# Performance work log

Hardware: AMD Instinct MI355X
Metric: run time of the kernel (lower is better)

## Reference

```python
import jax, jax.numpy as jnp
import numpy as np

D_MODEL = 1024
N_HEADS = 16
HEAD_DIM = D_MODEL // N_HEADS  # 64; used only as softmax scale in windowed path
WINDOW = 128


def _window_starts(seq_len, window):
    # Faithful to the torch loop: stride = window//2, last window right-aligned.
    starts = []
    for i in range(0, seq_len, window // 2):
        end = min(i + window, seq_len)
        starts.append(max(0, end - window))
        if end == seq_len:
            break
    return np.asarray(starts, dtype=np.int32)


def setup_inputs() -> dict:
    key = jax.random.key(0)
    ks = jax.random.split(key, 9)
    B, S = 4, 4096
    sc = 1.0 / np.sqrt(D_MODEL)
    return {
        "x": jax.random.normal(ks[0], (B, S, D_MODEL), jnp.float32),
        "Wq": jax.random.normal(ks[1], (D_MODEL, D_MODEL), jnp.float32) * sc,
        "bq": jax.random.normal(ks[2], (D_MODEL,), jnp.float32) * 0.02,
        "Wk": jax.random.normal(ks[3], (D_MODEL, D_MODEL), jnp.float32) * sc,
        "bk": jax.random.normal(ks[4], (D_MODEL,), jnp.float32) * 0.02,
        "Wv": jax.random.normal(ks[5], (D_MODEL, D_MODEL), jnp.float32) * sc,
        "bv": jax.random.normal(ks[6], (D_MODEL,), jnp.float32) * 0.02,
        "Wo": jax.random.normal(ks[7], (D_MODEL, D_MODEL), jnp.float32) * sc,
        "bo": jax.random.normal(ks[8], (D_MODEL,), jnp.float32) * 0.02,
    }


def reference(x, Wq, bq, Wk, bk, Wv, bv, Wo, bo):
    B, S, D = x.shape
    q = x @ Wq + bq  # [B,S,D]
    k = x @ Wk + bk
    v = x @ Wv + bv

    # Overlapping sliding windows (heads merged, as in the original windowed path).
    starts = _window_starts(S, WINDOW)                      # [W]
    idx = starts[:, None] + np.arange(WINDOW)[None, :]      # [W, w] static
    idx_j = jnp.asarray(idx)
    qw = q[:, idx_j]  # [B, W, w, D]
    kw = k[:, idx_j]
    vw = v[:, idx_j]
    scores = jnp.einsum('bwqd,bwkd->bwqk', qw, kw) / np.sqrt(HEAD_DIM)
    attn = jax.nn.softmax(scores, axis=-1)
    out_w = jnp.einsum('bwqk,bwkd->bwqd', attn, vw)         # [B, W, w, D]

    # Overlap-add then average by coverage counts.
    flat_idx = idx.reshape(-1)
    out = jnp.zeros((B, S, D), x.dtype).at[:, flat_idx].add(
        out_w.reshape(B, -1, D))
    counts = jnp.zeros((S,), x.dtype).at[flat_idx].add(1.0)
    out = out / counts[None, :, None]

    return out @ Wo + bo
```

## Files before the change

### kernel.cpp

```cpp
#include <hip/hip_runtime.h>
#include <stdint.h>
#include <stddef.h>

#define D_MODEL 1024
#define SEQ     4096
#define BATCH   4
#define MTOT    (BATCH*SEQ)
#define NWIN    63

typedef __bf16 bf16;
typedef __bf16 bf16x8 __attribute__((ext_vector_type(8)));
typedef __bf16 bf16x4 __attribute__((ext_vector_type(4)));
typedef float  floatx4 __attribute__((ext_vector_type(4)));

__device__ __forceinline__ void async_ld16(const void* g, void* l) {
  __builtin_amdgcn_global_load_lds(
      (const __attribute__((address_space(1))) unsigned int*)g,
      (__attribute__((address_space(3))) unsigned int*)l,
      16, 0, 0);
}


__global__ __launch_bounds__(256)
void cvt_x_kernel(const float* __restrict__ x, bf16* __restrict__ xb)
{
  const int i = blockIdx.x * 256 + threadIdx.x;
  const float4 v = ((const float4*)x)[i];
  bf16x4 o = { (bf16)v.x, (bf16)v.y, (bf16)v.z, (bf16)v.w };
  ((bf16x4*)xb)[i] = o;
}

__global__ __launch_bounds__(256)
void cvt_wt_kernel(const float* __restrict__ W0, const float* __restrict__ W1,
                   const float* __restrict__ W2, const float* __restrict__ W3,
                   bf16* __restrict__ wt)
{
  __shared__ float tile[32][33];
  const float* Wsel = (blockIdx.z == 0) ? W0 : (blockIdx.z == 1) ? W1
                    : (blockIdx.z == 2) ? W2 : W3;
  bf16* Wt = wt + (size_t)blockIdx.z * D_MODEL * D_MODEL;
  const int tx = threadIdx.x & 31, ty = threadIdx.x >> 5;
  const int tn = blockIdx.x * 32, tk = blockIdx.y * 32;
#pragma unroll
  for (int j = 0; j < 32; j += 8)
    tile[ty + j][tx] = Wsel[(size_t)(tk + ty + j) * D_MODEL + (tn + tx)];
  __syncthreads();
#pragma unroll
  for (int j = 0; j < 32; j += 8)
    Wt[(size_t)(tn + ty + j) * D_MODEL + (tk + tx)] = (bf16)tile[tx][ty + j];
}

__device__ __forceinline__ void stage_tile(const bf16* __restrict__ Ab,
                                           const bf16* __restrict__ Bb,
                                           bf16* As, bf16* Bs, int t, int buf,
                                           int w, int l)
{
  const int k0 = t << 5;
  bf16* Ad = As + buf * 8192;
  bf16* Bd = Bs + buf * 8192;
#pragma unroll
  for (int i = 0; i < 2; ++i) {
    const int f = w * 2 + i;
    async_ld16(Ab + (size_t)(f * 16) * D_MODEL + k0, Ad + f * 512 + l * 8);
    async_ld16(Bb + (size_t)(f * 16) * D_MODEL + k0, Bd + f * 512 + l * 8);
  }
}

__device__ __forceinline__ void gemm_core_256(const bf16* __restrict__ A,
                                              const bf16* __restrict__ Bt,
                                              int m0, int n0,
                                              bf16* As, bf16* Bs,
                                              floatx4 (&acc)[8][4],
                                              int w, int l)
{
  const int ll = l & 15, lh = l >> 4;
  const int wm = w >> 2, wn = w & 3;
  const bf16* Ab = A  + (size_t)(m0 + ll) * D_MODEL + lh * 8;
  const bf16* Bb = Bt + (size_t)(n0 + ll) * D_MODEL + lh * 8;

  stage_tile(Ab, Bb, As, Bs, 0, 0, w, l);
  stage_tile(Ab, Bb, As, Bs, 1, 1, w, l);

  for (int t = 0; t < 32; ++t) {
    if (t < 31) asm volatile("s_waitcnt vmcnt(4)" ::: "memory");
    else        asm volatile("s_waitcnt vmcnt(0)" ::: "memory");
    __builtin_amdgcn_s_barrier();
    __builtin_amdgcn_sched_barrier(0);
    const bf16* Ac = As + (t & 1) * 8192;
    const bf16* Bc = Bs + (t & 1) * 8192;
    bf16x8 af[8], bfr[4];
#pragma unroll
    for (int mt = 0; mt < 8; ++mt)
      af[mt]  = *(const bf16x8*)&Ac[(wm * 8 + mt) * 512 + l * 8];
#pragma unroll
    for (int nt = 0; nt < 4; ++nt)
      bfr[nt] = *(const bf16x8*)&Bc[(wn * 4 + nt) * 512 + l * 8];
    __builtin_amdgcn_s_setprio(1);
#pragma unroll
    for (int mt = 0; mt < 8; ++mt)
#pragma unroll
      for (int nt = 0; nt < 4; ++nt)
        acc[mt][nt] = __builtin_amdgcn_mfma_f32_16x16x32_bf16(af[mt], bfr[nt], acc[mt][nt], 0, 0, 0);
    __builtin_amdgcn_s_setprio(0);
    __builtin_amdgcn_sched_barrier(0);
    __builtin_amdgcn_s_barrier();
    __builtin_amdgcn_sched_barrier(0);
    if (t + 2 < 32) stage_tile(Ab, Bb, As, Bs, t + 2, t & 1, w, l);
  }
}

__global__ __launch_bounds__(512, 2)
void gemm_qkv(const bf16* __restrict__ A, const bf16* __restrict__ Bt,
              const float* __restrict__ bq, const float* __restrict__ bk,
              const float* __restrict__ bv,
              bf16* __restrict__ qo, bf16* __restrict__ ko, bf16* __restrict__ vto)
{
  __shared__ __attribute__((aligned(16))) bf16 As[16384];
  __shared__ __attribute__((aligned(16))) bf16 Bs[16384];
  const int tid = threadIdx.x;
  const int w = tid >> 6, l = tid & 63;
  const int ll = l & 15, lh = l >> 4;
  const int wm = w >> 2, wn = w & 3;

  const int idx = blockIdx.x;
  const int xcd = idx & 7;
  const int local = idx >> 3;
  const int msub = local & 7;
  const int nblk = local >> 3;
  const int mblk = xcd * 8 + msub;
  const int m0 = mblk * 256, n0 = nblk * 256;

  floatx4 acc[8][4];
#pragma unroll
  for (int i = 0; i < 8; ++i)
#pragma unroll
    for (int j = 0; j < 4; ++j) acc[i][j] = (floatx4)0.f;

  gemm_core_256(A, Bt, m0, n0, As, Bs, acc, w, l);

  const int sel = n0 >> 10;
  const int ncl = n0 & 1023;
  const float* bias = (sel == 0) ? bq : (sel == 1) ? bk : bv;

#pragma unroll
  for (int mt = 0; mt < 8; ++mt) {
#pragma unroll
    for (int nt = 0; nt < 4; ++nt) {
      const int colL = ncl + wn * 64 + nt * 16 + ll;
      const float bvv = bias[colL];
#pragma unroll
      for (int r = 0; r < 4; ++r) {
        const int row = m0 + wm * 128 + mt * 16 + lh * 4 + r;
        const float v = acc[mt][nt][r] + bvv;
        if (sel == 0) {
          qo[(size_t)row * D_MODEL + colL] = (bf16)v;
        } else if (sel == 1) {
          ko[(size_t)row * D_MODEL + colL] = (bf16)v;
        } else {
          const int bb = row >> 12, s = row & 4095;
          vto[((size_t)bb * D_MODEL + colL) * SEQ + s] = (bf16)v;
        }
      }
    }
  }
}

__global__ __launch_bounds__(512, 2)
void gemm_out(const bf16* __restrict__ A, const bf16* __restrict__ Bt,
              const float* __restrict__ bias, float* __restrict__ C)
{
  __shared__ __attribute__((aligned(16))) bf16 As[16384];
  __shared__ __attribute__((aligned(16))) bf16 Bs[16384];
  const int tid = threadIdx.x;
  const int w = tid >> 6, l = tid & 63;
  const int ll = l & 15, lh = l >> 4;
  const int wm = w >> 2, wn = w & 3;

  const int idx = blockIdx.x;
  const int xcd = idx & 7;
  const int local = idx >> 3;
  const int msub = local & 7;
  const int nblk = local >> 3;
  const int mblk = xcd * 8 + msub;
  const int m0 = mblk * 256, n0 = nblk * 256;

  floatx4 acc[8][4];
#pragma unroll
  for (int i = 0; i < 8; ++i)
#pragma unroll
    for (int j = 0; j < 4; ++j) acc[i][j] = (floatx4)0.f;

  gemm_core_256(A, Bt, m0, n0, As, Bs, acc, w, l);

#pragma unroll
  for (int mt = 0; mt < 8; ++mt) {
#pragma unroll
    for (int nt = 0; nt < 4; ++nt) {
      const int col = n0 + wn * 64 + nt * 16 + ll;
      const float bvv = bias[col];
#pragma unroll
      for (int r = 0; r < 4; ++r) {
        const int row = m0 + wm * 128 + mt * 16 + lh * 4 + r;
        C[(size_t)row * D_MODEL + col] = acc[mt][nt][r] + bvv;
      }
    }
  }
}

__global__ __launch_bounds__(256)
void qk_softmax(const bf16* __restrict__ qb, const bf16* __restrict__ kb,
                bf16* __restrict__ Pg)
{
  __shared__ __attribute__((aligned(16))) bf16 As[8192];
  __shared__ __attribute__((aligned(16))) bf16 Bs[16384];
  __shared__ float redM[4][64];
  __shared__ float redS[4][64];

  const int tid = threadIdx.x;
  const int w = tid >> 6, l = tid & 63, ll = l & 15, lh = l >> 4;
  const int wh = blockIdx.x;
  const int win = wh >> 1, half = wh & 1;
  const int b = blockIdx.y;

  const bf16* Aq = qb + ((size_t)b * SEQ + win * 64 + half * 64) * D_MODEL
                 + (size_t)ll * D_MODEL + lh * 8;
  const bf16* Ak = kb + ((size_t)b * SEQ + win * 64) * D_MODEL
                 + (size_t)ll * D_MODEL + lh * 8;

  floatx4 acc[4][2];
#pragma unroll
  for (int i = 0; i < 4; ++i)
#pragma unroll
    for (int j = 0; j < 2; ++j) acc[i][j] = (floatx4)0.f;

  auto stage = [&](int t, int buf) {
    const int c0 = t << 6;
    bf16* Ad = As + buf * 4096;
    bf16* Bd = Bs + buf * 8192;
#pragma unroll
    for (int i = 0; i < 2; ++i) {
      const int f = w * 2 + i;
      const int mt = f & 3, kk = f >> 2;
      async_ld16(Aq + (size_t)(mt * 16) * D_MODEL + (c0 + kk * 32),
                 Ad + f * 512 + l * 8);
    }
#pragma unroll
    for (int i = 0; i < 4; ++i) {
      const int f = w * 4 + i;
      const int mt = f & 7, kk = f >> 3;
      async_ld16(Ak + (size_t)(mt * 16) * D_MODEL + (c0 + kk * 32),
                 Bd + f * 512 + l * 8);
    }
  };

  stage(0, 0);
  stage(1, 1);

  for (int t = 0; t < 16; ++t) {
    if (t < 15) asm volatile("s_waitcnt vmcnt(6)" ::: "memory");
    else        asm volatile("s_waitcnt vmcnt(0)" ::: "memory");
    __builtin_amdgcn_s_barrier();
    __builtin_amdgcn_sched_barrier(0);
    const bf16* Ac = As + (t & 1) * 4096;
    const bf16* Bc = Bs + (t & 1) * 8192;
#pragma unroll
    for (int kk = 0; kk < 2; ++kk) {
      bf16x8 af[4], bfr[2];
#pragma unroll
      for (int tt = 0; tt < 4; ++tt)
        af[tt]  = *(const bf16x8*)&Ac[(kk * 4 + tt) * 512 + l * 8];
#pragma unroll
      for (int tt = 0; tt < 2; ++tt)
        bfr[tt] = *(const bf16x8*)&Bc[(kk * 8 + w * 2 + tt) * 512 + l * 8];
      __builtin_amdgcn_s_setprio(1);
#pragma unroll
      for (int mt = 0; mt < 4; ++mt)
#pragma unroll
        for (int nt = 0; nt < 2; ++nt)
          acc[mt][nt] = __builtin_amdgcn_mfma_f32_16x16x32_bf16(af[mt], bfr[nt], acc[mt][nt], 0, 0, 0);
      __builtin_amdgcn_s_setprio(0);
    }
    __builtin_amdgcn_sched_barrier(0);
    __builtin_amdgcn_s_barrier();
    __builtin_amdgcn_sched_barrier(0);
    if (t + 2 < 16) stage(t + 2, t & 1);
  }

#pragma unroll
  for (int mt = 0; mt < 4; ++mt)
#pragma unroll
    for (int nt = 0; nt < 2; ++nt)
#pragma unroll
      for (int r = 0; r < 4; ++r) acc[mt][nt][r] *= 0.125f;

#pragma unroll
  for (int mt = 0; mt < 4; ++mt)
#pragma unroll
    for (int r = 0; r < 4; ++r) {
      float m = fmaxf(acc[mt][0][r], acc[mt][1][r]);
      m = fmaxf(m, __shfl_xor(m, 1));
      m = fmaxf(m, __shfl_xor(m, 2));
      m = fmaxf(m, __shfl_xor(m, 4));
      m = fmaxf(m, __shfl_xor(m, 8));
      if (ll == 0) redM[w][mt * 16 + lh * 4 + r] = m;
    }
  __syncthreads();

#pragma unroll
  for (int mt = 0; mt < 4; ++mt)
#pragma unroll
    for (int r = 0; r < 4; ++r) {
      const int row = mt * 16 + lh * 4 + r;
      const float m = fmaxf(fmaxf(redM[0][row], redM[1][row]),
                            fmaxf(redM[2][row], redM[3][row]));
      const float e0 = __expf(acc[mt][0][r] - m);
      const float e1 = __expf(acc[mt][1][r] - m);
      acc[mt][0][r] = e0; acc[mt][1][r] = e1;
      float s = e0 + e1;
      s += __shfl_xor(s, 1);
      s += __shfl_xor(s, 2);
      s += __shfl_xor(s, 4);
      s += __shfl_xor(s, 8);
      if (ll == 0) redS[w][row] = s;
    }
  __syncthreads();

  bf16* Pb = Pg + ((size_t)(b * NWIN + win) * 128 + half * 64) * 128;
#pragma unroll
  for (int mt = 0; mt < 4; ++mt)
#pragma unroll
    for (int r = 0; r < 4; ++r) {
      const int row = mt * 16 + lh * 4 + r;
      const float inv = 1.f / (redS[0][row] + redS[1][row] + redS[2][row] + redS[3][row]);
#pragma unroll
      for (int nt = 0; nt < 2; ++nt)
        Pb[(size_t)row * 128 + w * 32 + nt * 16 + ll] = (bf16)(acc[mt][nt][r] * inv);
    }
}

__global__ __launch_bounds__(256)
void pv_gather(const bf16* __restrict__ Pg, const bf16* __restrict__ vt,
               bf16* __restrict__ ab)
{
  __shared__ __attribute__((aligned(16))) bf16 As[4096];
  __shared__ __attribute__((aligned(16))) bf16 Bs[8192];

  const int tid = threadIdx.x;
  const int w = tid >> 6, l = tid & 63, ll = l & 15, lh = l >> 4;
  const int d0 = blockIdx.x * 128;
  const int h  = blockIdx.y;
  const int b  = blockIdx.z;

  int wseg[2], roff[2];
  int nseg = 0;
  if (h >= 1)        { wseg[nseg] = h - 1; roff[nseg] = 64; ++nseg; }
  if (h <= NWIN - 1) { wseg[nseg] = h;     roff[nseg] = 0;  ++nseg; }
  const float scale = (nseg == 2) ? 0.5f : 1.0f;

  floatx4 acc[4][2];
#pragma unroll
  for (int i = 0; i < 4; ++i)
#pragma unroll
    for (int j = 0; j < 2; ++j) acc[i][j] = (floatx4)0.f;

  for (int sg = 0; sg < nseg; ++sg) {
    const bf16* Pseg = Pg + ((size_t)(b * NWIN + wseg[sg]) * 128 + roff[sg]) * 128;
    const bf16* Vseg = vt + ((size_t)b * D_MODEL + d0) * SEQ + wseg[sg] * 64;
    for (int c0 = 0; c0 < 128; c0 += 64) {
#pragma unroll
      for (int i = 0; i < 2; ++i) {
        const int f = w * 2 + i;
        const int mt = f & 3, kk = f >> 2;
        async_ld16(Pseg + (size_t)(mt * 16 + ll) * 128 + (c0 + kk * 32 + lh * 8),
                   &As[f * 512 + l * 8]);
      }
#pragma unroll
      for (int i = 0; i < 4; ++i) {
        const int f = w * 4 + i;
        const int mt = f & 7, kk = f >> 3;
        async_ld16(Vseg + (size_t)(mt * 16 + ll) * SEQ + (c0 + kk * 32 + lh * 8),
                   &Bs[f * 512 + l * 8]);
      }
      __syncthreads();
#pragma unroll
      for (int kk = 0; kk < 2; ++kk) {
        bf16x8 af[4], bfr[2];
#pragma unroll
        for (int t = 0; t < 4; ++t)
          af[t]  = *(const bf16x8*)&As[(kk * 4 + t) * 512 + l * 8];
#pragma unroll
        for (int t = 0; t < 2; ++t)
          bfr[t] = *(const bf16x8*)&Bs[(kk * 8 + w * 2 + t) * 512 + l * 8];
#pragma unroll
        for (int mt = 0; mt < 4; ++mt)
#pragma unroll
          for (int nt = 0; nt < 2; ++nt)
            acc[mt][nt] = __builtin_amdgcn_mfma_f32_16x16x32_bf16(af[mt], bfr[nt], acc[mt][nt], 0, 0, 0);
      }
      __syncthreads();
    }
  }

#pragma unroll
  for (int mt = 0; mt < 4; ++mt)
#pragma unroll
    for (int nt = 0; nt < 2; ++nt)
#pragma unroll
      for (int r = 0; r < 4; ++r) {
        const int row = h * 64 + mt * 16 + lh * 4 + r;
        const int col = d0 + w * 32 + nt * 16 + ll;
        ab[((size_t)b * SEQ + row) * D_MODEL + col] = (bf16)(acc[mt][nt][r] * scale);
      }
}

extern "C" void kernel_launch(void* const* d_in, const int* in_sizes, int n_in,
                              void* d_out, int out_size, void* d_ws, size_t ws_size,
                              hipStream_t stream)
{
  (void)in_sizes; (void)n_in; (void)out_size;

  const float* x  = (const float*)d_in[0];
  const float* Wq = (const float*)d_in[1];
  const float* bq = (const float*)d_in[2];
  const float* Wk = (const float*)d_in[3];
  const float* bk = (const float*)d_in[4];
  const float* Wv = (const float*)d_in[5];
  const float* bv = (const float*)d_in[6];
  const float* Wo = (const float*)d_in[7];
  const float* bo = (const float*)d_in[8];

  if (ws_size < (size_t)176160768) return;
  char* ws = (char*)d_ws;
  bf16* xb = (bf16*)(ws);
  bf16* pb = (bf16*)(ws);
  bf16* wt = (bf16*)(ws + 33554432);
  bf16* qb = (bf16*)(ws + 41943040);
  bf16* kb = (bf16*)(ws + 75497472);
  bf16* vt = (bf16*)(ws + 109051904);
  bf16* ab = (bf16*)(ws + 142606336);

  cvt_x_kernel<<<16384, 256, 0, stream>>>(x, xb);
  cvt_wt_kernel<<<dim3(32, 32, 4), 256, 0, stream>>>(Wq, Wk, Wv, Wo, wt);

  gemm_qkv<<<768, 512, 0, stream>>>(xb, wt, bq, bk, bv, qb, kb, vt);

  qk_softmax<<<dim3(126, BATCH), 256, 0, stream>>>(qb, kb, pb);
  pv_gather<<<dim3(8, 64, BATCH), 256, 0, stream>>>(pb, vt, ab);

  gemm_out<<<256, 512, 0, stream>>>(ab, wt + 3145728, bo, (float*)d_out);
}
```

Baseline: 441.5 us.

## Triple-buffer GEMM LDS stages and interleave loads with split MFMA phases

Replaces the double-buffered GEMM main loop with a three-buffer pipeline. Each k-step is split into two halves that interleave async global-to-LDS loads, LDS fragment reads and MFMA bursts, and the trailing barrier that guarded buffer reuse is dropped. The goal is better overlap of memory traffic with matrix math and fewer stalls per iteration. LDS use grows from 64KB to 96KB per block, which may prevent two blocks per CU as the launch bounds request and so lower occupancy.

New measurement: 499.5 us. +13.1%, slower.

```diff
diff --git a/kernel.cpp b/kernel.cpp
--- a/kernel.cpp
+++ b/kernel.cpp
@@ -50,62 +50,70 @@
     Wt[(size_t)(tn + ty + j) * D_MODEL + (tk + tx)] = (bf16)tile[tx][ty + j];
 }
 
-__device__ __forceinline__ void stage_tile(const bf16* __restrict__ Ab,
-                                           const bf16* __restrict__ Bb,
-                                           bf16* As, bf16* Bs, int t, int buf,
-                                           int w, int l)
-{
-  const int k0 = t << 5;
-  bf16* Ad = As + buf * 8192;
-  bf16* Bd = Bs + buf * 8192;
-#pragma unroll
-  for (int i = 0; i < 2; ++i) {
-    const int f = w * 2 + i;
-    async_ld16(Ab + (size_t)(f * 16) * D_MODEL + k0, Ad + f * 512 + l * 8);
-    async_ld16(Bb + (size_t)(f * 16) * D_MODEL + k0, Bd + f * 512 + l * 8);
-  }
-}
-
-__device__ __forceinline__ void gemm_core_256(const bf16* __restrict__ A,
-                                              const bf16* __restrict__ Bt,
-                                              int m0, int n0,
-                                              bf16* As, bf16* Bs,
-                                              floatx4 (&acc)[8][4],
-                                              int w, int l)
+__device__ __forceinline__ void gemm_core_3b(const bf16* __restrict__ A,
+                                             const bf16* __restrict__ Bt,
+                                             int m0, int n0,
+                                             bf16* As, bf16* Bs,
+                                             floatx4 (&acc)[8][4],
+                                             int w, int l)
 {
   const int ll = l & 15, lh = l >> 4;
   const int wm = w >> 2, wn = w & 3;
   const bf16* Ab = A  + (size_t)(m0 + ll) * D_MODEL + lh * 8;
   const bf16* Bb = Bt + (size_t)(n0 + ll) * D_MODEL + lh * 8;
 
-  stage_tile(Ab, Bb, As, Bs, 0, 0, w, l);
-  stage_tile(Ab, Bb, As, Bs, 1, 1, w, l);
+  auto stage_unit = [&](int t, int u, int b) {
+    const int k0 = t << 5;
+    const int f = u * 8 + w;
+    async_ld16(Ab + (size_t)(f * 16) * D_MODEL + k0, As + b * 8192 + f * 512 + l * 8);
+    async_ld16(Bb + (size_t)(f * 16) * D_MODEL + k0, Bs + b * 8192 + f * 512 + l * 8);
+  };
+
+  stage_unit(0, 0, 0); stage_unit(0, 1, 0);
+  stage_unit(1, 0, 1); stage_unit(1, 1, 1);
+  asm volatile("s_waitcnt vmcnt(4)" ::: "memory");
+  __builtin_amdgcn_sched_barrier(0);
+  __builtin_amdgcn_s_barrier();
+  __builtin_amdgcn_sched_barrier(0);
 
   for (int t = 0; t < 32; ++t) {
-    if (t < 31) asm volatile("s_waitcnt vmcnt(4)" ::: "memory");
-    else        asm volatile("s_waitcnt vmcnt(0)" ::: "memory");
-    __builtin_amdgcn_s_barrier();
-    __builtin_amdgcn_sched_barrier(0);
-    const bf16* Ac = As + (t & 1) * 8192;
-    const bf16* Bc = Bs + (t & 1) * 8192;
-    bf16x8 af[8], bfr[4];
-#pragma unroll
-    for (int mt = 0; mt < 8; ++mt)
-      af[mt]  = *(const bf16x8*)&Ac[(wm * 8 + mt) * 512 + l * 8];
-#pragma unroll
-    for (int nt = 0; nt < 4; ++nt)
-      bfr[nt] = *(const bf16x8*)&Bc[(wn * 4 + nt) * 512 + l * 8];
-    __builtin_amdgcn_s_setprio(1);
-#pragma unroll
-    for (int mt = 0; mt < 8; ++mt)
-#pragma unroll
-      for (int nt = 0; nt < 4; ++nt)
-        acc[mt][nt] = __builtin_amdgcn_mfma_f32_16x16x32_bf16(af[mt], bfr[nt], acc[mt][nt], 0, 0, 0);
-    __builtin_amdgcn_s_setprio(0);
-    __builtin_amdgcn_sched_barrier(0);
-    __builtin_amdgcn_s_barrier();
-    __builtin_amdgcn_sched_barrier(0);
-    if (t + 2 < 32) stage_tile(Ab, Bb, As, Bs, t + 2, t & 1, w, l);
+    const bf16* Ac = As + (t % 3) * 8192;
+    const bf16* Bc = Bs + (t % 3) * 8192;
+    const int bn = (t + 2) % 3;
+    bf16x8 bfr[4];
+#pragma unroll
+    for (int p = 0; p < 2; ++p) {
+      if (t + 2 < 32) stage_unit(t + 2, p, bn);
+      if (p == 0) {
+#pragma unroll
+        for (int nt = 0; nt < 4; ++nt)
+          bfr[nt] = *(const bf16x8*)&Bc[(wn * 4 + nt) * 512 + l * 8];
+      }
+      bf16x8 af[4];
+#pragma unroll
+      for (int j = 0; j < 4; ++j)
+        af[j] = *(const bf16x8*)&Ac[(wm * 8 + p * 4 + j) * 512 + l * 8];
+      __builtin_amdgcn_sched_barrier(0);
+      __builtin_amdgcn_s_barrier();
+      asm volatile("s_waitcnt lgkmcnt(0)" ::: "memory");
+      __builtin_amdgcn_sched_barrier(0);
+      __builtin_amdgcn_s_setprio(1);
+#pragma unroll
+      for (int j = 0; j < 4; ++j)
+#pragma unroll
+        for (int nt = 0; nt < 4; ++nt)
+          acc[p * 4 + j][nt] = __builtin_amdgcn_mfma_f32_16x16x32_bf16(
+              af[j], bfr[nt], acc[p * 4 + j][nt], 0, 0, 0);
+      __builtin_amdgcn_s_setprio(0);
+      __builtin_amdgcn_sched_barrier(0);
+      if (p == 1) {
+        if (t + 2 < 32)      asm volatile("s_waitcnt vmcnt(4)" ::: "memory");
+        else if (t + 1 < 32) asm volatile("s_waitcnt vmcnt(0)" ::: "memory");
+        __builtin_amdgcn_sched_barrier(0);
+      }
+      __builtin_amdgcn_s_barrier();
+      __builtin_amdgcn_sched_barrier(0);
+    }
   }
 }
 
@@ -115,8 +123,8 @@
               const float* __restrict__ bv,
               bf16* __restrict__ qo, bf16* __restrict__ ko, bf16* __restrict__ vto)
 {
-  __shared__ __attribute__((aligned(16))) bf16 As[16384];
-  __shared__ __attribute__((aligned(16))) bf16 Bs[16384];
+  __shared__ __attribute__((aligned(16))) bf16 As[24576];
+  __shared__ __attribute__((aligned(16))) bf16 Bs[24576];
   const int tid = threadIdx.x;
   const int w = tid >> 6, l = tid & 63;
   const int ll = l & 15, lh = l >> 4;
@@ -136,7 +144,7 @@
 #pragma unroll
     for (int j = 0; j < 4; ++j) acc[i][j] = (floatx4)0.f;
 
-  gemm_core_256(A, Bt, m0, n0, As, Bs, acc, w, l);
+  gemm_core_3b(A, Bt, m0, n0, As, Bs, acc, w, l);
 
   const int sel = n0 >> 10;
   const int ncl = n0 & 1023;
@@ -169,8 +177,8 @@
 void gemm_out(const bf16* __restrict__ A, const bf16* __restrict__ Bt,
               const float* __restrict__ bias, float* __restrict__ C)
 {
-  __shared__ __attribute__((aligned(16))) bf16 As[16384];
-  __shared__ __attribute__((aligned(16))) bf16 Bs[16384];
+  __shared__ __attribute__((aligned(16))) bf16 As[24576];
+  __shared__ __attribute__((aligned(16))) bf16 Bs[24576];
   const int tid = threadIdx.x;
   const int w = tid >> 6, l = tid & 63;
   const int ll = l & 15, lh = l >> 4;
@@ -190,7 +198,7 @@
 #pragma unroll
     for (int j = 0; j < 4; ++j) acc[i][j] = (floatx4)0.f;
 
-  gemm_core_256(A, Bt, m0, n0, As, Bs, acc, w, l);
+  gemm_core_3b(A, Bt, m0, n0, As, Bs, acc, w, l);
 
 #pragma unroll
   for (int mt = 0; mt < 8; ++mt) {
```
